# Optimization experiments

Measured on AMD Instinct MI355X. Metric: run time of the kernel, lower is better.

## Reference

```python
import jax, jax.numpy as jnp
import numpy as np
from jax import lax

HID, WID, DAT = 16, 64, 2
B, L = 512, 256
MAX_STEPS = 12          # bounded adaptive-step budget (replaces diffrax while_loop)
T1 = 1.0
RTOL, ATOL = 1e-2, 1e-4  # diffrax.PIDController(rtol=0.01, atol=0.0001)
SAFETY, FMIN, FMAX = 0.9, 0.2, 10.0

# Tsit5 Butcher tableau
A21 = 0.161
A31, A32 = -0.008480655492356989, 0.335480655492357
A41, A42, A43 = 2.8971530571054935, -6.359448489975075, 4.3622954328695815
A51, A52, A53, A54 = 5.325864828439257, -11.748883564062828, 7.4955393428898365, -0.09249506636175525
A61, A62, A63, A64, A65 = 5.86145544294642, -12.92096931784711, 8.159367898576159, -0.071584973281401, -0.028269050394068383
B1, B2, B3, B4, B5, B6 = 0.09646076681806523, 0.01, 0.4798896504144996, 1.379008574103742, -3.290069515436081, 2.324710524099774
E1, E2, E3, E4, E5, E6, E7 = (-0.00178001105222577714, -0.0008164344596567469, 0.007880878010261995,
                              -0.1447110071732629, 0.5823571654525552, -0.45808210592918697, 0.015151515151515152)


def setup_inputs() -> dict:
    key = jax.random.key(0)
    ks = jax.random.split(key, 12)
    def lin(k, out_d, in_d):
        return (jax.random.normal(k, (out_d, in_d), jnp.float32) / np.sqrt(in_d)).astype(jnp.float32)
    return {
        "x_seq": jax.random.normal(ks[0], (B, L, DAT), jnp.float32),
        "W0": lin(ks[1], WID, HID), "b0": jnp.zeros((WID,), jnp.float32),
        "W1": lin(ks[2], WID, WID), "b1": jnp.zeros((WID,), jnp.float32),
        "W2": lin(ks[3], WID, WID), "b2": jnp.zeros((WID,), jnp.float32),
        "W3": lin(ks[4], HID, WID), "b3": jnp.zeros((HID,), jnp.float32),
        "Wih": lin(ks[5], 3 * HID, DAT), "Whh": lin(ks[6], 3 * HID, HID),
        "bih": jnp.zeros((3 * HID,), jnp.float32), "bn": jnp.zeros((HID,), jnp.float32),
        "Wp": lin(ks[7], 1, HID), "bp": jnp.zeros((1,), jnp.float32),
    }


def _mlp(y, W0, b0, W1, b1, W2, b2, W3, b3):
    # ODEFunc: tanh MLP 16 -> 64 -> 64 -> 64 -> 16 (depth=3)
    h = jnp.tanh(y @ W0.T + b0)
    h = jnp.tanh(h @ W1.T + b1)
    h = jnp.tanh(h @ W2.T + b2)
    return h @ W3.T + b3


def _ode_solve(y0, mlp_p):
    # Adaptive Tsit5 with I-controller over t in [0, 1], dt0=1, per-sample step sizes.
    f = lambda y: _mlp(y, *mlp_p)
    Bn = y0.shape[0]
    t0 = jnp.zeros((Bn, 1), y0.dtype)
    dt0 = jnp.ones((Bn, 1), y0.dtype)

    def step(carry, _):
        t, y, dt = carry
        done = t >= T1 - 1e-7
        dtc = jnp.where(done, jnp.ones_like(dt), jnp.minimum(dt, T1 - t))
        k1 = f(y)
        k2 = f(y + dtc * (A21 * k1))
        k3 = f(y + dtc * (A31 * k1 + A32 * k2))
        k4 = f(y + dtc * (A41 * k1 + A42 * k2 + A43 * k3))
        k5 = f(y + dtc * (A51 * k1 + A52 * k2 + A53 * k3 + A54 * k4))
        k6 = f(y + dtc * (A61 * k1 + A62 * k2 + A63 * k3 + A64 * k4 + A65 * k5))
        y_new = y + dtc * (B1 * k1 + B2 * k2 + B3 * k3 + B4 * k4 + B5 * k5 + B6 * k6)
        k7 = f(y_new)
        y_err = dtc * (E1 * k1 + E2 * k2 + E3 * k3 + E4 * k4 + E5 * k5 + E6 * k6 + E7 * k7)
        scale = ATOL + RTOL * jnp.maximum(jnp.abs(y), jnp.abs(y_new))
        err = jnp.sqrt(jnp.mean((y_err / scale) ** 2, axis=-1, keepdims=True))  # [B,1]
        upd = (~done) & (err <= 1.0)
        y = jnp.where(upd, y_new, y)
        t = jnp.where(upd, t + dtc, t)
        factor = jnp.clip(SAFETY * jnp.maximum(err, 1e-10) ** (-0.2), FMIN, FMAX)
        dt = jnp.where(done, dt, dtc * factor)
        return (t, y, dt), None

    (_, yF, _), _ = lax.scan(step, (t0, y0, dt0), None, length=MAX_STEPS)
    return yF


def _gru(x, h, Wih, Whh, bih, bn):
    # equinox GRUCell semantics
    ig = x @ Wih.T + bih
    hg = h @ Whh.T
    ir, iz, inew = jnp.split(ig, 3, axis=-1)
    hr, hz, hn = jnp.split(hg, 3, axis=-1)
    r = jax.nn.sigmoid(ir + hr)
    z = jax.nn.sigmoid(iz + hz)
    n = jnp.tanh(inew + r * (hn + bn))
    return n + z * (h - n)


def reference(x_seq, W0, b0, W1, b1, W2, b2, W3, b3, Wih, Whh, bih, bn, Wp, bp):
    Bn = x_seq.shape[0]
    mlp_p = (W0, b0, W1, b1, W2, b2, W3, b3)
    h0 = jnp.zeros((Bn, HID), x_seq.dtype)

    def body(h, xk):
        h_ev = _ode_solve(h, mlp_p)          # evolve hidden state with ODE
        h_up = _gru(xk, h_ev, Wih, Whh, bih, bn)  # GRU observation update
        return h_up, None

    hF, _ = lax.scan(body, h0, jnp.swapaxes(x_seq, 0, 1))  # scan over time [L,B,D]
    return hF @ Wp.T + bp  # [B, 1]
```

## Files before the change

kernel.cpp:

```cpp
#include <hip/hip_runtime.h>
#include <math.h>


namespace {
constexpr int LSEQ = 256;

typedef float f32x2 __attribute__((ext_vector_type(2)));

__device__ __forceinline__ f32x2 mk2(float a, float b) {
    f32x2 r; r.x = a; r.y = b; return r;
}
__device__ __forceinline__ f32x2 fma2(f32x2 a, f32x2 b, f32x2 c) {
    return __builtin_elementwise_fma(a, b, c);
}

__device__ __forceinline__ float tanh_f(float x) {
    float e = exp2f(x * 2.8853900817779268f);
    return 1.0f - 2.0f * __builtin_amdgcn_rcpf(e + 1.0f);
}
__device__ __forceinline__ float sigm_f(float x) {
    return __builtin_amdgcn_rcpf(1.0f + exp2f(x * -1.4426950408889634f));
}
}

extern "C" __global__ void __launch_bounds__(64, 1)
odern_kernel(const float* __restrict__ x_seq,
             const float* __restrict__ W0, const float* __restrict__ b0,
             const float* __restrict__ W1, const float* __restrict__ b1,
             const float* __restrict__ W2, const float* __restrict__ b2,
             const float* __restrict__ W3, const float* __restrict__ b3,
             const float* __restrict__ Wih, const float* __restrict__ Whh,
             const float* __restrict__ bih, const float* __restrict__ bn,
             const float* __restrict__ Wp, const float* __restrict__ bp,
             float* __restrict__ out)
{
    const int j   = threadIdx.x;
    const int b   = blockIdx.x;
    const int i16 = j & 15;

    __shared__ __align__(16) float s_in[16];
    __shared__ __align__(16) float s_hA[64];
    __shared__ __align__(16) float s_hB[64];
    __shared__ __align__(16) float s_x[2 * LSEQ];
    __shared__ float s_ig[48];
    __shared__ float s_hg[48];

    {
        const float4* xv = (const float4*)(x_seq + (long)b * (2 * LSEQ));
        float4 t0 = xv[j];
        float4 t1 = xv[j + 64];
        ((float4*)s_x)[j]      = t0;
        ((float4*)s_x)[j + 64] = t1;
    }

    f32x2 w0v[8], w1v[32], w2v[32], w3v[8], whv[8];
    {
        const float4* p = (const float4*)(W0 + j * 16);
        #pragma unroll
        for (int q = 0; q < 4; ++q) { float4 u = p[q];
            w0v[2*q] = mk2(u.x, u.y); w0v[2*q+1] = mk2(u.z, u.w); }
    }
    {
        const float4* p = (const float4*)(W1 + j * 64);
        #pragma unroll
        for (int q = 0; q < 16; ++q) { float4 u = p[q];
            w1v[2*q] = mk2(u.x, u.y); w1v[2*q+1] = mk2(u.z, u.w); }
    }
    {
        const float4* p = (const float4*)(W2 + j * 64);
        #pragma unroll
        for (int q = 0; q < 16; ++q) { float4 u = p[q];
            w2v[2*q] = mk2(u.x, u.y); w2v[2*q+1] = mk2(u.z, u.w); }
    }
    {
        const float4* p = (const float4*)(W3 + i16 * 64 + (j >> 4) * 16);
        #pragma unroll
        for (int q = 0; q < 4; ++q) { float4 u = p[q];
            w3v[2*q] = mk2(u.x, u.y); w3v[2*q+1] = mk2(u.z, u.w); }
    }
    const int jg = (j < 48) ? j : 47;
    {
        const float4* p = (const float4*)(Whh + jg * 16);
        #pragma unroll
        for (int q = 0; q < 4; ++q) { float4 u = p[q];
            whv[2*q] = mk2(u.x, u.y); whv[2*q+1] = mk2(u.z, u.w); }
    }
    const float wih0 = Wih[jg * 2], wih1 = Wih[jg * 2 + 1], bihj = bih[jg];
    const float bs0 = b0[j], bs1 = b1[j], bs2 = b2[j];
    const float b3r = b3[i16], bnr = bn[i16], wpr = Wp[i16];
    __syncthreads();

    auto dot64 = [&](const float4* p4, const f32x2* wv, float bias) -> float {
        f32x2 a0 = mk2(bias, 0.f), a1 = mk2(0.f, 0.f),
              a2 = mk2(0.f, 0.f),  a3 = mk2(0.f, 0.f);
        #pragma unroll
        for (int q = 0; q < 16; q += 2) {
            float4 u = p4[q];
            a0 = fma2(wv[2*q],   mk2(u.x, u.y), a0);
            a1 = fma2(wv[2*q+1], mk2(u.z, u.w), a1);
            float4 v = p4[q+1];
            a2 = fma2(wv[2*q+2], mk2(v.x, v.y), a2);
            a3 = fma2(wv[2*q+3], mk2(v.z, v.w), a3);
        }
        f32x2 s = (a0 + a1) + (a2 + a3);
        return s.x + s.y;
    };
    auto dot16 = [&](const float4* p4, const f32x2* wv, float bias) -> float {
        f32x2 a0 = mk2(bias, 0.f), a1 = mk2(0.f, 0.f);
        float4 u = p4[0];
        a0 = fma2(wv[0], mk2(u.x, u.y), a0);
        a1 = fma2(wv[1], mk2(u.z, u.w), a1);
        float4 v = p4[1];
        a0 = fma2(wv[2], mk2(v.x, v.y), a0);
        a1 = fma2(wv[3], mk2(v.z, v.w), a1);
        float4 w = p4[2];
        a0 = fma2(wv[4], mk2(w.x, w.y), a0);
        a1 = fma2(wv[5], mk2(w.z, w.w), a1);
        float4 z = p4[3];
        a0 = fma2(wv[6], mk2(z.x, z.y), a0);
        a1 = fma2(wv[7], mk2(z.z, z.w), a1);
        f32x2 s = a0 + a1;
        return s.x + s.y;
    };

    auto mlp = [&](float ys) -> float {
        if (j < 16) s_in[j] = ys;
        __syncthreads();
        float a = tanh_f(dot16((const float4*)s_in, w0v, bs0));
        s_hA[j] = a;
        __syncthreads();
        float a1 = tanh_f(dot64((const float4*)s_hA, w1v, bs1));
        s_hB[j] = a1;
        __syncthreads();
        float a2 = tanh_f(dot64((const float4*)s_hB, w2v, bs2));
        s_hA[j] = a2;
        __syncthreads();
        float p = dot16((const float4*)s_hA + (j >> 4) * 4, w3v, 0.f);
        p += __shfl_xor(p, 16);
        p += __shfl_xor(p, 32);
        __syncthreads();
        return p + b3r;
    };

    const float A21 = 0.161f;
    const float A31 = -0.008480655492356989f, A32 = 0.335480655492357f;
    const float A41 = 2.8971530571054935f, A42 = -6.359448489975075f, A43 = 4.3622954328695815f;
    const float A51 = 5.325864828439257f, A52 = -11.748883564062828f, A53 = 7.4955393428898365f, A54 = -0.09249506636175525f;
    const float A61 = 5.86145544294642f, A62 = -12.92096931784711f, A63 = 8.159367898576159f, A64 = -0.071584973281401f, A65 = -0.028269050394068383f;
    const float B1 = 0.09646076681806523f, B2 = 0.01f, B3 = 0.4798896504144996f,
                B4 = 1.379008574103742f, B5 = -3.290069515436081f, B6 = 2.324710524099774f;
    const float E1 = -0.00178001105222577714f, E2 = -0.0008164344596567469f,
                E3 = 0.007880878010261995f, E4 = -0.1447110071732629f,
                E5 = 0.5823571654525552f, E6 = -0.45808210592918697f, E7 = 0.015151515151515152f;
    const float TDONE = (float)(1.0 - 1e-7);

    float y = 0.0f;

    #pragma unroll 1
    for (int l = 0; l < LSEQ; ++l) {
        float t = 0.f, dt = 1.f;
        #pragma unroll 1
        for (int it = 0; it < 12; ++it) {
            if (t >= TDONE) break;
            float dtc = fminf(dt, 1.0f - t);
            float k1 = mlp(y);
            float k2 = mlp(fmaf(dtc, A21 * k1, y));
            float k3 = mlp(fmaf(dtc, A31*k1 + A32*k2, y));
            float k4 = mlp(fmaf(dtc, A41*k1 + A42*k2 + A43*k3, y));
            float k5 = mlp(fmaf(dtc, A51*k1 + A52*k2 + A53*k3 + A54*k4, y));
            float k6 = mlp(fmaf(dtc, A61*k1 + A62*k2 + A63*k3 + A64*k4 + A65*k5, y));
            float ynew = fmaf(dtc, B1*k1 + B2*k2 + B3*k3 + B4*k4 + B5*k5 + B6*k6, y);
            float k7 = mlp(ynew);
            float yerr = dtc * (E1*k1 + E2*k2 + E3*k3 + E4*k4 + E5*k5 + E6*k6 + E7*k7);
            float sc = fmaf(0.01f, fmaxf(fabsf(y), fabsf(ynew)), 1e-4f);
            float e = yerr / sc;
            float e2 = e * e;
            e2 += __shfl_xor(e2, 1); e2 += __shfl_xor(e2, 2);
            e2 += __shfl_xor(e2, 4); e2 += __shfl_xor(e2, 8);
            float err = sqrtf(e2 * 0.0625f);
            if (err <= 1.0f) { y = ynew; t += dtc; }
            float fac = 0.9f * exp2f(-0.2f * log2f(fmaxf(err, 1e-10f)));
            fac = fminf(fmaxf(fac, 0.2f), 10.0f);
            dt = dtc * fac;
        }
        float x0 = s_x[2*l], x1 = s_x[2*l + 1];
        if (j < 16) s_in[j] = y;
        __syncthreads();
        float hg = dot16((const float4*)s_in, whv, 0.f);
        float ig = fmaf(wih0, x0, fmaf(wih1, x1, bihj));
        if (j < 48) { s_ig[j] = ig; s_hg[j] = hg; }
        __syncthreads();
        float ir = s_ig[i16], iz = s_ig[16+i16], in_ = s_ig[32+i16];
        float hr = s_hg[i16], hz = s_hg[16+i16], hn = s_hg[32+i16];
        float r = sigm_f(ir + hr);
        float z = sigm_f(iz + hz);
        float n = tanh_f(fmaf(r, hn + bnr, in_));
        y = n + z * (y - n);
        __syncthreads();
    }

    float pv = y * wpr;
    pv += __shfl_xor(pv, 1); pv += __shfl_xor(pv, 2);
    pv += __shfl_xor(pv, 4); pv += __shfl_xor(pv, 8);
    if (j == 0) out[b] = pv + bp[0];
}

extern "C" void kernel_launch(void* const* d_in, const int* in_sizes, int n_in,
                              void* d_out, int out_size, void* d_ws, size_t ws_size,
                              hipStream_t stream)
{
    odern_kernel<<<dim3(512), dim3(64), 0, stream>>>(
        (const float*)d_in[0],
        (const float*)d_in[1],  (const float*)d_in[2],
        (const float*)d_in[3],  (const float*)d_in[4],
        (const float*)d_in[5],  (const float*)d_in[6],
        (const float*)d_in[7],  (const float*)d_in[8],
        (const float*)d_in[9],  (const float*)d_in[10],
        (const float*)d_in[11], (const float*)d_in[12],
        (const float*)d_in[13], (const float*)d_in[14],
        (float*)d_out);
}
```

Measured before the change: 1.662 ms.

## Move MLP weights to swizzled LDS, use readlane inputs and FSAL k1 reuse

Moves W1/W2 from per-thread registers into XOR-swizzled shared memory to cut VGPR pressure. The 16-wide input layers (W0, Whh) now broadcast y with readlane instead of an LDS round trip. Since the block is a single wavefront, __syncthreads is replaced with compiler memory fences. It also adds the Tsit5 first-same-as-last property, reusing k7 as the next k1 after an accepted step, which saves one MLP evaluation per step. The risks are extra LDS traffic for the weights on every layer and reliance on single-wave lockstep for correctness.

```diff
diff --git a/kernel.cpp b/kernel.cpp
--- a/kernel.cpp
+++ b/kernel.cpp
@@ -13,6 +13,10 @@
 __device__ __forceinline__ f32x2 fma2(f32x2 a, f32x2 b, f32x2 c) {
     return __builtin_elementwise_fma(a, b, c);
 }
+__device__ __forceinline__ float RL(float v, int k) {
+    return __uint_as_float(__builtin_amdgcn_readlane(__float_as_uint(v), k));
+}
+#define LDSFENCE() asm volatile("" ::: "memory")
 
 __device__ __forceinline__ float tanh_f(float x) {
     float e = exp2f(x * 2.8853900817779268f);
@@ -37,8 +41,10 @@
     const int j   = threadIdx.x;
     const int b   = blockIdx.x;
     const int i16 = j & 15;
-
-    __shared__ __align__(16) float s_in[16];
+    const int xr4 = (j & 7) << 2;
+
+    __shared__ __align__(16) float s_w1[64 * 64];
+    __shared__ __align__(16) float s_w2[64 * 64];
     __shared__ __align__(16) float s_hA[64];
     __shared__ __align__(16) float s_hB[64];
     __shared__ __align__(16) float s_x[2 * LSEQ];
@@ -52,25 +58,23 @@
         ((float4*)s_x)[j]      = t0;
         ((float4*)s_x)[j + 64] = t1;
     }
-
-    f32x2 w0v[8], w1v[32], w2v[32], w3v[8], whv[8];
+    {
+        const float4* g1 = (const float4*)(W1 + j * 64);
+        const float4* g2 = (const float4*)(W2 + j * 64);
+        #pragma unroll
+        for (int q = 0; q < 16; ++q) {
+            *(float4*)(s_w1 + j * 64 + ((4 * q) ^ xr4)) = g1[q];
+            *(float4*)(s_w2 + j * 64 + ((4 * q) ^ xr4)) = g2[q];
+        }
+    }
+
+    float w0s[16], whs[16];
+    f32x2 w3v[8];
     {
         const float4* p = (const float4*)(W0 + j * 16);
         #pragma unroll
         for (int q = 0; q < 4; ++q) { float4 u = p[q];
-            w0v[2*q] = mk2(u.x, u.y); w0v[2*q+1] = mk2(u.z, u.w); }
-    }
-    {
-        const float4* p = (const float4*)(W1 + j * 64);
-        #pragma unroll
-        for (int q = 0; q < 16; ++q) { float4 u = p[q];
-            w1v[2*q] = mk2(u.x, u.y); w1v[2*q+1] = mk2(u.z, u.w); }
-    }
-    {
-        const float4* p = (const float4*)(W2 + j * 64);
-        #pragma unroll
-        for (int q = 0; q < 16; ++q) { float4 u = p[q];
-            w2v[2*q] = mk2(u.x, u.y); w2v[2*q+1] = mk2(u.z, u.w); }
+            w0s[4*q]=u.x; w0s[4*q+1]=u.y; w0s[4*q+2]=u.z; w0s[4*q+3]=u.w; }
     }
     {
         const float4* p = (const float4*)(W3 + i16 * 64 + (j >> 4) * 16);
@@ -83,30 +87,33 @@
         const float4* p = (const float4*)(Whh + jg * 16);
         #pragma unroll
         for (int q = 0; q < 4; ++q) { float4 u = p[q];
-            whv[2*q] = mk2(u.x, u.y); whv[2*q+1] = mk2(u.z, u.w); }
+            whs[4*q]=u.x; whs[4*q+1]=u.y; whs[4*q+2]=u.z; whs[4*q+3]=u.w; }
     }
     const float wih0 = Wih[jg * 2], wih1 = Wih[jg * 2 + 1], bihj = bih[jg];
     const float bs0 = b0[j], bs1 = b1[j], bs2 = b2[j];
     const float b3r = b3[i16], bnr = bn[i16], wpr = Wp[i16];
     __syncthreads();
 
-    auto dot64 = [&](const float4* p4, const f32x2* wv, float bias) -> float {
+    auto dot64w = [&](const float* wl, const float4* act, float bias) -> float {
+        const float* wrow = wl + j * 64;
         f32x2 a0 = mk2(bias, 0.f), a1 = mk2(0.f, 0.f),
               a2 = mk2(0.f, 0.f),  a3 = mk2(0.f, 0.f);
         #pragma unroll
         for (int q = 0; q < 16; q += 2) {
-            float4 u = p4[q];
-            a0 = fma2(wv[2*q],   mk2(u.x, u.y), a0);
-            a1 = fma2(wv[2*q+1], mk2(u.z, u.w), a1);
-            float4 v = p4[q+1];
-            a2 = fma2(wv[2*q+2], mk2(v.x, v.y), a2);
-            a3 = fma2(wv[2*q+3], mk2(v.z, v.w), a3);
+            float4 w4 = *(const float4*)(wrow + ((4 * q) ^ xr4));
+            float4 av = act[q];
+            a0 = fma2(mk2(w4.x, w4.y), mk2(av.x, av.y), a0);
+            a1 = fma2(mk2(w4.z, w4.w), mk2(av.z, av.w), a1);
+            float4 w5 = *(const float4*)(wrow + ((4 * (q + 1)) ^ xr4));
+            float4 au = act[q + 1];
+            a2 = fma2(mk2(w5.x, w5.y), mk2(au.x, au.y), a2);
+            a3 = fma2(mk2(w5.z, w5.w), mk2(au.z, au.w), a3);
         }
         f32x2 s = (a0 + a1) + (a2 + a3);
         return s.x + s.y;
     };
-    auto dot16 = [&](const float4* p4, const f32x2* wv, float bias) -> float {
-        f32x2 a0 = mk2(bias, 0.f), a1 = mk2(0.f, 0.f);
+    auto dot16pk = [&](const float4* p4, const f32x2* wv) -> float {
+        f32x2 a0 = mk2(0.f, 0.f), a1 = mk2(0.f, 0.f);
         float4 u = p4[0];
         a0 = fma2(wv[0], mk2(u.x, u.y), a0);
         a1 = fma2(wv[1], mk2(u.z, u.w), a1);
@@ -124,21 +131,27 @@
     };
 
     auto mlp = [&](float ys) -> float {
-        if (j < 16) s_in[j] = ys;
-        __syncthreads();
-        float a = tanh_f(dot16((const float4*)s_in, w0v, bs0));
+        float t0 = bs0, t1 = 0.f, t2 = 0.f, t3 = 0.f;
+        #pragma unroll
+        for (int k = 0; k < 16; k += 4) {
+            t0 = fmaf(w0s[k + 0], RL(ys, k + 0), t0);
+            t1 = fmaf(w0s[k + 1], RL(ys, k + 1), t1);
+            t2 = fmaf(w0s[k + 2], RL(ys, k + 2), t2);
+            t3 = fmaf(w0s[k + 3], RL(ys, k + 3), t3);
+        }
+        float a = tanh_f((t0 + t2) + (t1 + t3));
         s_hA[j] = a;
-        __syncthreads();
-        float a1 = tanh_f(dot64((const float4*)s_hA, w1v, bs1));
+        LDSFENCE();
+        float a1 = tanh_f(dot64w(s_w1, (const float4*)s_hA, bs1));
         s_hB[j] = a1;
-        __syncthreads();
-        float a2 = tanh_f(dot64((const float4*)s_hB, w2v, bs2));
+        LDSFENCE();
+        float a2 = tanh_f(dot64w(s_w2, (const float4*)s_hB, bs2));
         s_hA[j] = a2;
-        __syncthreads();
-        float p = dot16((const float4*)s_hA + (j >> 4) * 4, w3v, 0.f);
+        LDSFENCE();
+        float p = dot16pk((const float4*)s_hA + (j >> 4) * 4, w3v);
         p += __shfl_xor(p, 16);
         p += __shfl_xor(p, 32);
-        __syncthreads();
+        LDSFENCE();
         return p + b3r;
     };
 
@@ -159,11 +172,11 @@
     #pragma unroll 1
     for (int l = 0; l < LSEQ; ++l) {
         float t = 0.f, dt = 1.f;
+        float k1 = mlp(y);
         #pragma unroll 1
         for (int it = 0; it < 12; ++it) {
             if (t >= TDONE) break;
             float dtc = fminf(dt, 1.0f - t);
-            float k1 = mlp(y);
             float k2 = mlp(fmaf(dtc, A21 * k1, y));
             float k3 = mlp(fmaf(dtc, A31*k1 + A32*k2, y));
             float k4 = mlp(fmaf(dtc, A41*k1 + A42*k2 + A43*k3, y));
@@ -178,25 +191,31 @@
             e2 += __shfl_xor(e2, 1); e2 += __shfl_xor(e2, 2);
             e2 += __shfl_xor(e2, 4); e2 += __shfl_xor(e2, 8);
             float err = sqrtf(e2 * 0.0625f);
-            if (err <= 1.0f) { y = ynew; t += dtc; }
+            if (err <= 1.0f) { y = ynew; t += dtc; k1 = k7; }
             float fac = 0.9f * exp2f(-0.2f * log2f(fmaxf(err, 1e-10f)));
             fac = fminf(fmaxf(fac, 0.2f), 10.0f);
             dt = dtc * fac;
         }
         float x0 = s_x[2*l], x1 = s_x[2*l + 1];
-        if (j < 16) s_in[j] = y;
-        __syncthreads();
-        float hg = dot16((const float4*)s_in, whv, 0.f);
+        float h0 = 0.f, h1 = 0.f, h2 = 0.f, h3 = 0.f;
+        #pragma unroll
+        for (int k = 0; k < 16; k += 4) {
+            h0 = fmaf(whs[k + 0], RL(y, k + 0), h0);
+            h1 = fmaf(whs[k + 1], RL(y, k + 1), h1);
+            h2 = fmaf(whs[k + 2], RL(y, k + 2), h2);
+            h3 = fmaf(whs[k + 3], RL(y, k + 3), h3);
+        }
+        float hg = (h0 + h2) + (h1 + h3);
         float ig = fmaf(wih0, x0, fmaf(wih1, x1, bihj));
         if (j < 48) { s_ig[j] = ig; s_hg[j] = hg; }
-        __syncthreads();
+        LDSFENCE();
         float ir = s_ig[i16], iz = s_ig[16+i16], in_ = s_ig[32+i16];
         float hr = s_hg[i16], hz = s_hg[16+i16], hn = s_hg[32+i16];
         float r = sigm_f(ir + hr);
         float z = sigm_f(iz + hz);
         float n = tanh_f(fmaf(r, hn + bnr, in_));
         y = n + z * (y - n);
-        __syncthreads();
+        LDSFENCE();
     }
 
     float pv = y * wpr;
```

Measured after the change: 1.835 ms. 10.4% more time.
